# Performance work log

Hardware: AMD Instinct MI355X
Metric: run time of the kernel (lower is better)

Reference implementation:

```python
import jax, jax.numpy as jnp
import numpy as np

N, D_IN, D_OUT = 16384, 64, 64
AVG_DEG = 32.0
L2_EPS = 1e-12  # torch F.normalize default eps


def setup_inputs() -> dict:
    key = jax.random.key(0)
    kx, ka, kw, kb = jax.random.split(key, 4)
    X = jax.random.normal(kx, (N, D_IN), dtype=jnp.float32)
    # binary adjacency with avg degree ~AVG_DEG (module treats adj as 0/1 mask)
    adj = (jax.random.uniform(ka, (N, N)) < (AVG_DEG / N)).astype(jnp.float32)
    # nn.Linear(2*D_IN, D_OUT): store W as (2*D_IN, D_OUT) for x @ W + b
    bound = 1.0 / np.sqrt(2 * D_IN)
    W = jax.random.uniform(kw, (2 * D_IN, D_OUT), dtype=jnp.float32, minval=-bound, maxval=bound)
    b = jax.random.uniform(kb, (D_OUT,), dtype=jnp.float32, minval=-bound, maxval=bound)
    return {"X": X, "adj": adj, "W": W, "b": b}


def reference(X, adj, W, b):
    # eval-mode mean aggregation: h_neigh = (adj + I) @ X / clamp(rowsum(adj + I), 1)
    # (adj + I) @ X == adj @ X + X, avoiding materializing the NxN identity.
    deg = jnp.clip(jnp.sum(adj, axis=1, keepdims=True) + 1.0, 1.0, None)  # (N,1)
    h_neigh = (adj @ X + X) / deg                                          # (N,D)
    concat = jnp.concatenate([X, h_neigh], axis=1)                         # (N,2D)
    z = concat @ W + b                                                     # (N,O)
    out = jax.nn.relu(z)
    norm = jnp.linalg.norm(out, axis=1, keepdims=True)
    return out / jnp.maximum(norm, L2_EPS)
```

## Files before the change

### kernel.cpp

```cpp
#include <hip/hip_runtime.h>
#include <stdint.h>


#define NROWS   16384
#define DDIM    64
#define MAXNNZ  256
#define NBLOCKS 4096
#define PIPE    8

typedef uint32_t u32x4 __attribute__((ext_vector_type(4)));

__global__ __launch_bounds__(256, 4) void sage_fused(
    const float* __restrict__ X,
    const float* __restrict__ adj,
    const float* __restrict__ W,
    const float* __restrict__ bias,
    float* __restrict__ out)
{
    __shared__ int   slist[4][MAXNNZ];
    __shared__ int   scnt[4];
    __shared__ float scat[4][2 * DDIM];

    const int tid  = threadIdx.x;
    const int lane = tid & 63;
    const int w    = tid >> 6;
    const int row  = blockIdx.x * 4 + w;

    const float bv = bias[lane];

    if (lane == 0) scnt[w] = 0;
    __builtin_amdgcn_wave_barrier();

    const int start = (row * 37 + (row >> 6) * 13) & 63;
    const u32x4* rowp = reinterpret_cast<const u32x4*>(adj + (size_t)row * NROWS);

    u32x4 buf[PIPE];
#pragma unroll
    for (int i = 0; i < PIPE; ++i)
        buf[i] = rowp[((start + i) & 63) * 64 + lane];

#pragma unroll 1
    for (int so = 0; so < 64; so += PIPE) {
#pragma unroll
        for (int i = 0; i < PIPE; ++i) {
            const int s  = so + i;
            const int ss = (start + s) & 63;
            const u32x4 vv = buf[i];
            if (vv.x | vv.y | vv.z | vv.w) {
                const int base = (ss * 64 + lane) * 4;
                const uint32_t w4[4] = { vv.x, vv.y, vv.z, vv.w };
#pragma unroll
                for (int j = 0; j < 4; ++j) {
                    if (w4[j]) {
                        const int p = atomicAdd(&scnt[w], 1);
                        if (p < MAXNNZ) slist[w][p] = base + j;
                    }
                }
            }
            if (so + PIPE < 64) {
                const int sn = (start + s + PIPE) & 63;
                buf[i] = rowp[sn * 64 + lane];
            }
        }
    }
    __builtin_amdgcn_wave_barrier();

    const int nnz = scnt[w];
    const int cn  = (nnz < MAXNNZ) ? nnz : MAXNNZ;

    float acc = 0.0f;
    int k = 0;
    for (; k + 4 <= cn; k += 4) {
        const int j0 = slist[w][k], j1 = slist[w][k + 1];
        const int j2 = slist[w][k + 2], j3 = slist[w][k + 3];
        const float a0 = X[(size_t)j0 * DDIM + lane];
        const float a1 = X[(size_t)j1 * DDIM + lane];
        const float a2 = X[(size_t)j2 * DDIM + lane];
        const float a3 = X[(size_t)j3 * DDIM + lane];
        acc += (a0 + a1) + (a2 + a3);
    }
    for (; k < cn; ++k) acc += X[(size_t)slist[w][k] * DDIM + lane];

    const float xi = X[(size_t)row * DDIM + lane];
    const float h  = (acc + xi) / ((float)nnz + 1.0f);
    scat[w][lane]        = xi;
    scat[w][DDIM + lane] = h;
    __builtin_amdgcn_wave_barrier();

    float z0 = bv, z1 = 0.0f, z2 = 0.0f, z3 = 0.0f;
#pragma unroll 8
    for (int kk = 0; kk < 2 * DDIM; kk += 4) {
        z0 = fmaf(scat[w][kk + 0], W[(kk + 0) * DDIM + lane], z0);
        z1 = fmaf(scat[w][kk + 1], W[(kk + 1) * DDIM + lane], z1);
        z2 = fmaf(scat[w][kk + 2], W[(kk + 2) * DDIM + lane], z2);
        z3 = fmaf(scat[w][kk + 3], W[(kk + 3) * DDIM + lane], z3);
    }
    float z = (z0 + z1) + (z2 + z3);
    z = fmaxf(z, 0.0f);

    float s2 = z * z;
#pragma unroll
    for (int off = 32; off >= 1; off >>= 1) s2 += __shfl_xor(s2, off);
    const float inv = 1.0f / fmaxf(sqrtf(s2), 1e-12f);
    out[(size_t)row * DDIM + lane] = z * inv;
}

extern "C" void kernel_launch(void* const* d_in, const int* in_sizes, int n_in,
                              void* d_out, int out_size, void* d_ws, size_t ws_size,
                              hipStream_t stream) {
    const float* X   = (const float*)d_in[0];
    const float* adj = (const float*)d_in[1];
    const float* W   = (const float*)d_in[2];
    const float* b   = (const float*)d_in[3];
    float* out = (float*)d_out;
    sage_fused<<<NBLOCKS, 256, 0, stream>>>(X, adj, W, b, out);
}
```

Before: 1.334 ms.

## Replace LDS atomic neighbor compaction with ballot/mbcnt chunk-mask compaction

The per-element LDS atomicAdd that compacts nonzero adjacency indices is replaced by a wave ballot plus mbcnt prefix, storing one packed entry per nonzero 16-byte chunk with a 4-bit mask built from the float 1.0 exponent bits. The gather loop decodes each chunk mask and counts nnz from it. It also raises the launch_bounds occupancy hint from 4 to 6 and changes the start-offset hash. The mask trick assumes adjacency values are exactly 0.0 or 1.0. The gather loop is no longer unrolled and has data-dependent branches, which may cost some memory-level parallelism.

After: 1.342 ms. No clear change (+0.6%).

```diff
diff --git a/kernel.cpp b/kernel.cpp
--- a/kernel.cpp
+++ b/kernel.cpp
@@ -2,23 +2,22 @@
 #include <stdint.h>
 
 
-#define NROWS   16384
-#define DDIM    64
-#define MAXNNZ  256
-#define NBLOCKS 4096
-#define PIPE    8
+#define NROWS    16384
+#define DDIM     64
+#define MAXCHUNK 256
+#define NBLOCKS  4096
+#define PIPE     8
 
 typedef uint32_t u32x4 __attribute__((ext_vector_type(4)));
 
-__global__ __launch_bounds__(256, 4) void sage_fused(
+__global__ __launch_bounds__(256, 6) void sage_fused(
     const float* __restrict__ X,
     const float* __restrict__ adj,
     const float* __restrict__ W,
     const float* __restrict__ bias,
     float* __restrict__ out)
 {
-    __shared__ int   slist[4][MAXNNZ];
-    __shared__ int   scnt[4];
+    __shared__ int   slist[4][MAXCHUNK];
     __shared__ float scat[4][2 * DDIM];
 
     const int tid  = threadIdx.x;
@@ -28,10 +27,7 @@
 
     const float bv = bias[lane];
 
-    if (lane == 0) scnt[w] = 0;
-    __builtin_amdgcn_wave_barrier();
-
-    const int start = (row * 37 + (row >> 6) * 13) & 63;
+    const int start = ((row * 7 + (row >> 4)) & 15) * 4;
     const u32x4* rowp = reinterpret_cast<const u32x4*>(adj + (size_t)row * NROWS);
 
     u32x4 buf[PIPE];
@@ -39,47 +35,49 @@
     for (int i = 0; i < PIPE; ++i)
         buf[i] = rowp[((start + i) & 63) * 64 + lane];
 
+    int cnt = 0;
 #pragma unroll 1
     for (int so = 0; so < 64; so += PIPE) {
 #pragma unroll
         for (int i = 0; i < PIPE; ++i) {
-            const int s  = so + i;
-            const int ss = (start + s) & 63;
+            const int g = (start + so + i) & 63;
             const u32x4 vv = buf[i];
-            if (vv.x | vv.y | vv.z | vv.w) {
-                const int base = (ss * 64 + lane) * 4;
-                const uint32_t w4[4] = { vv.x, vv.y, vv.z, vv.w };
-#pragma unroll
-                for (int j = 0; j < 4; ++j) {
-                    if (w4[j]) {
-                        const int p = atomicAdd(&scnt[w], 1);
-                        if (p < MAXNNZ) slist[w][p] = base + j;
-                    }
+            const bool nz = (vv.x | vv.y | vv.z | vv.w) != 0;
+            const uint64_t bal = __ballot(nz);
+            if (bal) {
+                const uint32_t m = ((vv.x >> 29) & 1u) | ((vv.y >> 28) & 2u)
+                                 | ((vv.z >> 27) & 4u) | ((vv.w >> 26) & 8u);
+                const int prefix = __builtin_amdgcn_mbcnt_hi(
+                    (uint32_t)(bal >> 32),
+                    __builtin_amdgcn_mbcnt_lo((uint32_t)bal, 0));
+                if (nz) {
+                    const int pos = cnt + prefix;
+                    if (pos < MAXCHUNK)
+                        slist[w][pos] = (((g << 6) + lane) << 4) | (int)m;
                 }
+                cnt += (int)__popcll(bal);
             }
-            if (so + PIPE < 64) {
-                const int sn = (start + s + PIPE) & 63;
-                buf[i] = rowp[sn * 64 + lane];
-            }
+            if (so + PIPE < 64)
+                buf[i] = rowp[((start + so + i + PIPE) & 63) * 64 + lane];
         }
     }
     __builtin_amdgcn_wave_barrier();
 
-    const int nnz = scnt[w];
-    const int cn  = (nnz < MAXNNZ) ? nnz : MAXNNZ;
+    const int cn = (cnt < MAXCHUNK) ? cnt : MAXCHUNK;
 
     float acc = 0.0f;
-    int k = 0;
-    for (; k + 4 <= cn; k += 4) {
-        const int j0 = slist[w][k], j1 = slist[w][k + 1];
-        const int j2 = slist[w][k + 2], j3 = slist[w][k + 3];
-        const float a0 = X[(size_t)j0 * DDIM + lane];
-        const float a1 = X[(size_t)j1 * DDIM + lane];
-        const float a2 = X[(size_t)j2 * DDIM + lane];
-        const float a3 = X[(size_t)j3 * DDIM + lane];
-        acc += (a0 + a1) + (a2 + a3);
+    int nnz = 0;
+    for (int k = 0; k < cn; ++k) {
+        const int e  = slist[w][k];
+        const int ci = e >> 4;
+        const uint32_t m = e & 15u;
+        nnz += __popc(m);
+        const float* xb = X + (size_t)ci * 4 * DDIM + lane;
+        if (m & 1u) acc += xb[0 * DDIM];
+        if (m & 2u) acc += xb[1 * DDIM];
+        if (m & 4u) acc += xb[2 * DDIM];
+        if (m & 8u) acc += xb[3 * DDIM];
     }
-    for (; k < cn; ++k) acc += X[(size_t)slist[w][k] * DDIM + lane];
 
     const float xi = X[(size_t)row * DDIM + lane];
     const float h  = (acc + xi) / ((float)nnz + 1.0f);
```
